# Kernel optimization log

Measured on AMD Instinct MI355X. Metric: run time of the kernel, lower is better.

## Reference

```python
import jax, jax.numpy as jnp
import numpy as np

IN_COUNT = 1024
OUT_COUNT = 1024
NUM_BASIS = 8
INPUT_ABS_MAX = 1.0
X_MIN = 0.0
X_MAX = 1.0
GAMMA_SCALE = 3.0
BATCH = 4096


def setup_inputs() -> dict:
    key = jax.random.key(0)
    k_x, k_c = jax.random.split(key)
    x = jax.random.normal(k_x, (BATCH, IN_COUNT), dtype=jnp.float32)
    coeffs = 0.01 * jax.random.normal(k_c, (OUT_COUNT, IN_COUNT, NUM_BASIS), dtype=jnp.float32)
    # fixed buffers
    centers_1d = jnp.linspace(X_MIN, X_MAX, NUM_BASIS)
    centers = jnp.broadcast_to(centers_1d[None, :], (IN_COUNT, NUM_BASIS)).astype(jnp.float32)
    delta = (X_MAX - X_MIN) / (NUM_BASIS - 1)
    gamma = GAMMA_SCALE / delta
    slopes = jnp.full((IN_COUNT, NUM_BASIS), gamma, dtype=jnp.float32)
    alpha = jnp.full((IN_COUNT,), (X_MAX - X_MIN) / (2.0 * INPUT_ABS_MAX), dtype=jnp.float32)
    beta = jnp.full((IN_COUNT,), 0.5 * (X_MIN + X_MAX), dtype=jnp.float32)
    return {"x": x, "coeffs": coeffs, "centers": centers, "slopes": slopes, "alpha": alpha, "beta": beta}


def reference(x, coeffs, centers, slopes, alpha, beta):
    # u: (B, in) affine transform with fixed alpha/beta
    u = alpha[None, :] * x + beta[None, :]
    # basis: (B, in, basis) = 0.5*(1+tanh(slope*(u - center)))
    basis = 0.5 * (1.0 + jnp.tanh(slopes[None, :, :] * (u[:, :, None] - centers[None, :, :])))
    # y[b,o] = sum_{i,m} coeffs[o,i,m] * basis[b,i,m]  (fused GEMM over in*basis)
    y = jnp.einsum('bim,oim->bo', basis, coeffs)
    return y
```

## Files before the change

kernel.cpp:

```cpp
#include <hip/hip_runtime.h>
#include <hip/hip_bf16.h>
#include <cstdint>
#include <cstddef>

#define BATCH 4096
#define INC   1024
#define OUTC  1024
#define NB    8
#define KDIM  (INC * NB)

#define BM 256
#define BN 256
#define BKB 64
#define SPLITS 4
#define KZ (KDIM / SPLITS)
#define KSTEPS (KZ / BKB)
#define GRID_BLOCKS ((OUTC / BN) * (BATCH / BM) * SPLITS)

#define EXPAND_BLOCKS  ((BATCH * INC) / 256)
#define QUANT_BLOCKS   OUTC
#define PREP_BLOCKS    (EXPAND_BLOCKS + QUANT_BLOCKS)

typedef int   v4i __attribute__((ext_vector_type(4)));
typedef char  v8c __attribute__((ext_vector_type(8)));
typedef short v8s __attribute__((ext_vector_type(8)));

__device__ __forceinline__ unsigned short f2bf(float f) {
  union { float f; unsigned u; } v; v.f = f;
  unsigned r = v.u + 0x7fffu + ((v.u >> 16) & 1u);
  return (unsigned short)(r >> 16);
}
__device__ __forceinline__ float bf2f(unsigned short h) {
  union { unsigned u; float f; } v; v.u = ((unsigned)h) << 16; return v.f;
}

__device__ __forceinline__ void gld16(const char* g, char* l) {
  __builtin_amdgcn_global_load_lds(
      (const __attribute__((address_space(1))) unsigned int*)g,
      (__attribute__((address_space(3))) unsigned int*)l, 16, 0, 0);
}

__global__ __launch_bounds__(256) void prep_kernel(
    const float* __restrict__ x, const float4* __restrict__ coeffs4,
    const float* __restrict__ centers, const float* __restrict__ slopes,
    const float* __restrict__ alpha, const float* __restrict__ beta,
    char* __restrict__ Ai8, int* __restrict__ Ci8i,
    float* __restrict__ maxrow, int* __restrict__ qcsum) {
  const int blk = blockIdx.x;
  const int tid = threadIdx.x;
  if (blk < EXPAND_BLOCKS) {
    const int idx = blk * 256 + tid;
    const int i = idx & (INC - 1);
    const float u = alpha[i] * x[idx] + beta[i];
    const float s0 = slopes[i * NB];
    const float c0 = centers[i * NB];
    const float c1 = centers[i * NB + 1];
    const float L2E2 = 2.8853900817779268f;
    const float a2 = L2E2 * s0;
    float e = __builtin_amdgcn_exp2f(a2 * (c0 - u));
    const float R = __builtin_amdgcn_exp2f(a2 * (c1 - c0));
    v8c q;
#pragma unroll
    for (int m = 0; m < 8; ++m) {
      float basis = __builtin_amdgcn_rcpf(1.0f + e);
      q[m] = (char)(int)rintf(basis * 254.0f - 127.0f);
      e *= R;
    }
    *(v8c*)(Ai8 + (size_t)idx * 8) = q;
  } else {
    const int o = blk - EXPAND_BLOCKS;
    const float4* row = coeffs4 + (size_t)o * (KDIM / 4);
    float4 v[8];
    float m = 0.0f;
#pragma unroll
    for (int j = 0; j < 8; ++j) {
      v[j] = row[tid + 256 * j];
      m = fmaxf(m, fmaxf(fmaxf(fabsf(v[j].x), fabsf(v[j].y)),
                         fmaxf(fabsf(v[j].z), fabsf(v[j].w))));
    }
#pragma unroll
    for (int off = 32; off; off >>= 1) m = fmaxf(m, __shfl_xor(m, off));
    __shared__ float wm[4];
    __shared__ int   wq[4];
    if ((tid & 63) == 0) wm[tid >> 6] = m;
    __syncthreads();
    const float M = fmaxf(fmaxf(fmaxf(wm[0], wm[1]), fmaxf(wm[2], wm[3])), 1e-30f);
    const float s = 127.0f / M;
    int qs = 0;
#pragma unroll
    for (int j = 0; j < 8; ++j) {
      int q0 = (int)rintf(v[j].x * s), q1 = (int)rintf(v[j].y * s);
      int q2 = (int)rintf(v[j].z * s), q3 = (int)rintf(v[j].w * s);
      Ci8i[(size_t)o * (KDIM / 4) + tid + 256 * j] =
          (q0 & 0xFF) | ((q1 & 0xFF) << 8) | ((q2 & 0xFF) << 16) | ((q3 & 0xFF) << 24);
      qs += q0 + q1 + q2 + q3;
    }
#pragma unroll
    for (int off = 32; off; off >>= 1) qs += __shfl_xor(qs, off);
    if ((tid & 63) == 0) wq[tid >> 6] = qs;
    __syncthreads();
    if (tid == 0) { maxrow[o] = M; qcsum[o] = wq[0] + wq[1] + wq[2] + wq[3]; }
  }
}

__global__ __launch_bounds__(512, 2) void gemm_kernel(
    const char* __restrict__ A, const char* __restrict__ C,
    unsigned short* __restrict__ partials) {
  __shared__ __align__(16) char As[3][BM * BKB];
  __shared__ __align__(16) char Bs[3][BN * BKB];

  const int id = (blockIdx.x & 7) * (GRID_BLOCKS / 8) + (blockIdx.x >> 3);
  const int z  = id >> 6;
  const int p  = id & 63;
  const int by = p >> 2;
  const int bx = p & 3;
  const int bm0 = by * BM;
  const int bn0 = bx * BN;
  const int kt0 = z * KZ;

  const int tid  = threadIdx.x;
  const int wave = tid >> 6;
  const int lane = tid & 63;
  const int quad = lane >> 4;
  const int lm   = lane & 15;
  const int wm   = (wave >> 2) * 128;
  const int wn   = (wave & 3) * 64;

  const int r4 = lane >> 2;
  const int gg = (lane & 3) ^ ((lane >> 3) & 3);

  const char* pA0 = A + (size_t)(bm0 + wave * 32 + r4) * KDIM + kt0 + gg * 16;
  const char* pB0 = C + (size_t)(bn0 + wave * 32 + r4) * KDIM + kt0 + gg * 16;
  const int lo = wave * 32 * BKB;

  const int kx   = (quad ^ ((lm >> 1) & 3)) * 16;
  const int aoff = (wm + lm) * BKB + kx;
  const int boff = (wn + lm) * BKB + kx;

  v4i acc[8][4] = {};
  v4i a0v[8], b0v[4], a1v[8], b1v[4];
  int srd = 0;
  int sst = 0;

#define STAGE_NEXT()                                                         \
  {                                                                          \
    _Pragma("unroll")                                                        \
    for (int j = 0; j < 2; ++j) {                                            \
      gld16(pA0 + (size_t)j * (16 * KDIM), As[sst] + lo + j * (16 * BKB));   \
      gld16(pB0 + (size_t)j * (16 * KDIM), Bs[sst] + lo + j * (16 * BKB));   \
    }                                                                        \
    pA0 += BKB; pB0 += BKB;                                                  \
    sst = (sst == 2) ? 0 : sst + 1;                                          \
  }

#define READS(AV, BV)                                                        \
  {                                                                          \
    const char* cA = As[srd] + aoff;                                         \
    const char* cB = Bs[srd] + boff;                                         \
    _Pragma("unroll")                                                        \
    for (int f = 0; f < 8; ++f) AV[f] = *(const v4i*)(cA + f * 16 * BKB);    \
    _Pragma("unroll")                                                        \
    for (int f = 0; f < 4; ++f) BV[f] = *(const v4i*)(cB + f * 16 * BKB);    \
    srd = (srd == 2) ? 0 : srd + 1;                                          \
  }

#define MFMA32(AV, BV)                                                       \
  {                                                                          \
    __builtin_amdgcn_s_setprio(1);                                           \
    _Pragma("unroll")                                                        \
    for (int fm = 0; fm < 8; ++fm)                                           \
      _Pragma("unroll")                                                      \
      for (int fn = 0; fn < 4; ++fn)                                         \
        acc[fm][fn] = __builtin_amdgcn_mfma_i32_16x16x64_i8(AV[fm], BV[fn], acc[fm][fn], 0, 0, 0); \
    __builtin_amdgcn_s_setprio(0);                                           \
  }

#define STEP(CA, CB, NA, NBV, VMS, LGS, DOREADS, DOSTAGE)                    \
  {                                                                          \
    if (DOREADS) {                                                           \
      asm volatile("s_waitcnt vmcnt(" VMS ")" ::: "memory");                 \
      __builtin_amdgcn_sched_barrier(0);                                     \
      __builtin_amdgcn_s_barrier();                                          \
      READS(NA, NBV);                                                        \
    }                                                                        \
    asm volatile("s_waitcnt lgkmcnt(" LGS ")" ::: "memory");                 \
    __builtin_amdgcn_sched_barrier(0);                                       \
    __builtin_amdgcn_s_barrier();                                            \
    if (DOSTAGE) STAGE_NEXT();                                               \
    MFMA32(CA, CB);                                                          \
  }

  STAGE_NEXT(); STAGE_NEXT(); STAGE_NEXT();
  asm volatile("s_waitcnt vmcnt(8)" ::: "memory");
  __builtin_amdgcn_sched_barrier(0);
  __builtin_amdgcn_s_barrier();
  READS(a0v, b0v);

  for (int i = 0; i < 14; ++i) {
    STEP(a0v, b0v, a1v, b1v, "4", "12", true, true);
    STEP(a1v, b1v, a0v, b0v, "4", "12", true, true);
  }
  STEP(a0v, b0v, a1v, b1v, "4", "12", true, true);
  STEP(a1v, b1v, a0v, b0v, "4", "12", true, false);
  STEP(a0v, b0v, a1v, b1v, "0", "12", true, false);
  STEP(a1v, b1v, a0v, b0v, "0", "0",  false, false);
#undef STEP
#undef MFMA32
#undef READS
#undef STAGE_NEXT

  unsigned short* out = partials + (size_t)z * BATCH * OUTC;
#pragma unroll
  for (int fm = 0; fm < 8; ++fm) {
    const int row0 = bm0 + wm + fm * 16 + quad * 4;
#pragma unroll
    for (int fn = 0; fn < 4; ++fn) {
      const int col = bn0 + wn + fn * 16 + lm;
#pragma unroll
      for (int r = 0; r < 4; ++r)
        out[(size_t)(row0 + r) * OUTC + col] = f2bf((float)acc[fm][fn][r]);
    }
  }
}

__global__ __launch_bounds__(256) void reduce_kernel(
    const unsigned short* __restrict__ P, const float* __restrict__ maxrow,
    const int* __restrict__ qcsum, float* __restrict__ out) {
  const size_t nel = (size_t)BATCH * OUTC;
  const size_t base = ((size_t)blockIdx.x * 256 + threadIdx.x) * 8;
  float s[8] = {};
#pragma unroll
  for (int t = 0; t < SPLITS; ++t) {
    v8s v = *(const v8s*)(P + t * nel + base);
#pragma unroll
    for (int j = 0; j < 8; ++j) s[j] += bf2f((unsigned short)v[j]);
  }
  const int o0 = (int)(base & (OUTC - 1));
  const float inv = 1.0f / 32258.0f;
#pragma unroll
  for (int j = 0; j < 8; ++j) {
    const float M = maxrow[o0 + j];
    const int   Q = qcsum[o0 + j];
    s[j] = M * (s[j] + 127.0f * (float)Q) * inv;
  }
  *(float4*)(out + base)     = float4{s[0], s[1], s[2], s[3]};
  *(float4*)(out + base + 4) = float4{s[4], s[5], s[6], s[7]};
}

extern "C" void kernel_launch(void* const* d_in, const int* in_sizes, int n_in,
                              void* d_out, int out_size, void* d_ws, size_t ws_size,
                              hipStream_t stream) {
  const float* x       = (const float*)d_in[0];
  const float* coeffs  = (const float*)d_in[1];
  const float* centers = (const float*)d_in[2];
  const float* slopes  = (const float*)d_in[3];
  const float* alpha   = (const float*)d_in[4];
  const float* beta    = (const float*)d_in[5];
  float* out = (float*)d_out;

  const size_t a_bytes    = (size_t)BATCH * KDIM;
  const size_t c_bytes    = (size_t)OUTC * KDIM;
  const size_t stat_bytes = OUTC * sizeof(float);
  const size_t qcs_bytes  = OUTC * sizeof(int);
  const size_t part_bytes = (size_t)SPLITS * BATCH * OUTC * 2;
  if (ws_size < a_bytes + c_bytes + stat_bytes + qcs_bytes + part_bytes) return;

  char*  Ai8    = (char*)d_ws;
  char*  Ci8    = Ai8 + a_bytes;
  float* maxrow = (float*)(Ci8 + c_bytes);
  int*   qcsum  = (int*)((char*)maxrow + stat_bytes);
  unsigned short* parts = (unsigned short*)((char*)qcsum + qcs_bytes);

  prep_kernel<<<PREP_BLOCKS, 256, 0, stream>>>(
      x, (const float4*)coeffs, centers, slopes, alpha, beta,
      Ai8, (int*)Ci8, maxrow, qcsum);

  gemm_kernel<<<GRID_BLOCKS, 512, 0, stream>>>(Ai8, Ci8, parts);

  reduce_kernel<<<(int)((size_t)BATCH * OUTC / 8 / 256), 256, 0, stream>>>(
      parts, maxrow, qcsum, out);
}
```

Before: 152.8 us.

## Interleave LDS reads and global loads with MFMA quarters; store partials in fragment layout

The GEMM main loop is split into four quarter-steps. Each quarter issues a few LDS fragment reads and one global-to-LDS load, then runs eight MFMAs, with fine-grained lgkmcnt gates and barriers. This is meant to overlap memory traffic with matrix math instead of doing all reads up front. The epilogue now writes bf16 partials in the native accumulator fragment layout as coalesced 16-byte stores, and the reduce kernel is rewritten to read that layout, transpose through shared memory, and write the output coalesced. The extra barriers per step add synchronisation cost, and the reduce grid shrinks to 512 blocks.

```diff
diff --git a/kernel.cpp b/kernel.cpp
--- a/kernel.cpp
+++ b/kernel.cpp
@@ -16,14 +16,15 @@
 #define KZ (KDIM / SPLITS)
 #define KSTEPS (KZ / BKB)
 #define GRID_BLOCKS ((OUTC / BN) * (BATCH / BM) * SPLITS)
+#define FRAG (16 * BKB)
 
 #define EXPAND_BLOCKS  ((BATCH * INC) / 256)
 #define QUANT_BLOCKS   OUTC
 #define PREP_BLOCKS    (EXPAND_BLOCKS + QUANT_BLOCKS)
 
-typedef int   v4i __attribute__((ext_vector_type(4)));
-typedef char  v8c __attribute__((ext_vector_type(8)));
-typedef short v8s __attribute__((ext_vector_type(8)));
+typedef int      v4i __attribute__((ext_vector_type(4)));
+typedef unsigned v4u __attribute__((ext_vector_type(4)));
+typedef char     v8c __attribute__((ext_vector_type(8)));
 
 __device__ __forceinline__ unsigned short f2bf(float f) {
   union { float f; unsigned u; } v; v.f = f;
@@ -105,7 +106,7 @@
 
 __global__ __launch_bounds__(512, 2) void gemm_kernel(
     const char* __restrict__ A, const char* __restrict__ C,
-    unsigned short* __restrict__ partials) {
+    unsigned* __restrict__ partials) {
   __shared__ __align__(16) char As[3][BM * BKB];
   __shared__ __align__(16) char Bs[3][BN * BKB];
 
@@ -138,113 +139,229 @@
   const int boff = (wn + lm) * BKB + kx;
 
   v4i acc[8][4] = {};
-  v4i a0v[8], b0v[4], a1v[8], b1v[4];
+  v4i xa[8], xb[4], ya[8], yb[4];
   int srd = 0;
   int sst = 0;
 
-#define STAGE_NEXT()                                                         \
-  {                                                                          \
-    _Pragma("unroll")                                                        \
-    for (int j = 0; j < 2; ++j) {                                            \
-      gld16(pA0 + (size_t)j * (16 * KDIM), As[sst] + lo + j * (16 * BKB));   \
-      gld16(pB0 + (size_t)j * (16 * KDIM), Bs[sst] + lo + j * (16 * BKB));   \
-    }                                                                        \
+#define STAGE_FULL()                                                         \
+  {                                                                          \
+    gld16(pA0,                     As[sst] + lo);                            \
+    gld16(pA0 + (size_t)16 * KDIM, As[sst] + lo + 16 * BKB);                 \
+    gld16(pB0,                     Bs[sst] + lo);                            \
+    gld16(pB0 + (size_t)16 * KDIM, Bs[sst] + lo + 16 * BKB);                 \
     pA0 += BKB; pB0 += BKB;                                                  \
     sst = (sst == 2) ? 0 : sst + 1;                                          \
   }
 
-#define READS(AV, BV)                                                        \
+#define MFMA8(AS, BS, FM0, FN0)                                              \
+  {                                                                          \
+    __builtin_amdgcn_s_setprio(1);                                           \
+    _Pragma("unroll")                                                        \
+    for (int fm = 0; fm < 4; ++fm)                                           \
+      _Pragma("unroll")                                                      \
+      for (int fn = 0; fn < 2; ++fn)                                         \
+        acc[FM0 + fm][FN0 + fn] = __builtin_amdgcn_mfma_i32_16x16x64_i8(     \
+            AS[FM0 + fm], BS[FN0 + fn], acc[FM0 + fm][FN0 + fn], 0, 0, 0);   \
+    __builtin_amdgcn_s_setprio(0);                                           \
+  }
+
+#define GATE(S)                                                              \
+  asm volatile("s_waitcnt lgkmcnt(" S ")" ::: "memory");                     \
+  __builtin_amdgcn_sched_barrier(0);
+
+#define HALF_MAIN(AX, BX, AY, BY)                                            \
   {                                                                          \
     const char* cA = As[srd] + aoff;                                         \
     const char* cB = Bs[srd] + boff;                                         \
-    _Pragma("unroll")                                                        \
-    for (int f = 0; f < 8; ++f) AV[f] = *(const v4i*)(cA + f * 16 * BKB);    \
-    _Pragma("unroll")                                                        \
-    for (int f = 0; f < 4; ++f) BV[f] = *(const v4i*)(cB + f * 16 * BKB);    \
+                                                                    \
+    AY[0] = *(const v4i*)(cA + 0 * FRAG);                                    \
+    AY[1] = *(const v4i*)(cA + 1 * FRAG);                                    \
+    AY[2] = *(const v4i*)(cA + 2 * FRAG);                                    \
+    gld16(pA0, As[sst] + lo);                                                \
+    asm volatile("s_waitcnt vmcnt(4)" ::: "memory");                         \
+    __builtin_amdgcn_sched_barrier(0);                                       \
+    __builtin_amdgcn_s_barrier();                                            \
+    GATE("3")                                                                \
+    MFMA8(AX, BX, 0, 0)                                                      \
+    __builtin_amdgcn_s_barrier();                                            \
+                                                                    \
+    AY[3] = *(const v4i*)(cA + 3 * FRAG);                                    \
+    BY[0] = *(const v4i*)(cB + 0 * FRAG);                                    \
+    BY[1] = *(const v4i*)(cB + 1 * FRAG);                                    \
+    gld16(pA0 + (size_t)16 * KDIM, As[sst] + lo + 16 * BKB);                 \
+    __builtin_amdgcn_s_barrier();                                            \
+    GATE("6")                                                                \
+    MFMA8(AX, BX, 0, 2)                                                      \
+    __builtin_amdgcn_s_barrier();                                            \
+                                                                    \
+    BY[2] = *(const v4i*)(cB + 2 * FRAG);                                    \
+    BY[3] = *(const v4i*)(cB + 3 * FRAG);                                    \
+    AY[4] = *(const v4i*)(cA + 4 * FRAG);                                    \
+    gld16(pB0, Bs[sst] + lo);                                                \
+    __builtin_amdgcn_s_barrier();                                            \
+    GATE("9")                                                                \
+    MFMA8(AX, BX, 4, 2)                                                      \
+    __builtin_amdgcn_s_barrier();                                            \
+                                                                    \
+    AY[5] = *(const v4i*)(cA + 5 * FRAG);                                    \
+    AY[6] = *(const v4i*)(cA + 6 * FRAG);                                    \
+    AY[7] = *(const v4i*)(cA + 7 * FRAG);                                    \
+    gld16(pB0 + (size_t)16 * KDIM, Bs[sst] + lo + 16 * BKB);                 \
+    __builtin_amdgcn_s_barrier();                                            \
+    GATE("0")                                                                \
+    MFMA8(AX, BX, 4, 0)                                                      \
+    __builtin_amdgcn_s_barrier();                                            \
+    pA0 += BKB; pB0 += BKB;                                                  \
+    sst = (sst == 2) ? 0 : sst + 1;                                          \
     srd = (srd == 2) ? 0 : srd + 1;                                          \
   }
 
-#define MFMA32(AV, BV)                                                       \
-  {                                                                          \
-    __builtin_amdgcn_s_setprio(1);                                           \
-    _Pragma("unroll")                                                        \
-    for (int fm = 0; fm < 8; ++fm)                                           \
-      _Pragma("unroll")                                                      \
-      for (int fn = 0; fn < 4; ++fn)                                         \
-        acc[fm][fn] = __builtin_amdgcn_mfma_i32_16x16x64_i8(AV[fm], BV[fn], acc[fm][fn], 0, 0, 0); \
-    __builtin_amdgcn_s_setprio(0);                                           \
-  }
-
-#define STEP(CA, CB, NA, NBV, VMS, LGS, DOREADS, DOSTAGE)                    \
-  {                                                                          \
-    if (DOREADS) {                                                           \
-      asm volatile("s_waitcnt vmcnt(" VMS ")" ::: "memory");                 \
-      __builtin_amdgcn_sched_barrier(0);                                     \
-      __builtin_amdgcn_s_barrier();                                          \
-      READS(NA, NBV);                                                        \
-    }                                                                        \
-    asm volatile("s_waitcnt lgkmcnt(" LGS ")" ::: "memory");                 \
+#define HALF_NOST(AX, BX, AY, BY, VMS)                                       \
+  {                                                                          \
+    const char* cA = As[srd] + aoff;                                         \
+    const char* cB = Bs[srd] + boff;                                         \
+    AY[0] = *(const v4i*)(cA + 0 * FRAG);                                    \
+    AY[1] = *(const v4i*)(cA + 1 * FRAG);                                    \
+    AY[2] = *(const v4i*)(cA + 2 * FRAG);                                    \
+    asm volatile("s_waitcnt vmcnt(" VMS ")" ::: "memory");                   \
     __builtin_amdgcn_sched_barrier(0);                                       \
     __builtin_amdgcn_s_barrier();                                            \
-    if (DOSTAGE) STAGE_NEXT();                                               \
-    MFMA32(CA, CB);                                                          \
-  }
-
-  STAGE_NEXT(); STAGE_NEXT(); STAGE_NEXT();
+    GATE("3")                                                                \
+    MFMA8(AX, BX, 0, 0)                                                      \
+    __builtin_amdgcn_s_barrier();                                            \
+    AY[3] = *(const v4i*)(cA + 3 * FRAG);                                    \
+    BY[0] = *(const v4i*)(cB + 0 * FRAG);                                    \
+    BY[1] = *(const v4i*)(cB + 1 * FRAG);                                    \
+    __builtin_amdgcn_s_barrier();                                            \
+    GATE("6")                                                                \
+    MFMA8(AX, BX, 0, 2)                                                      \
+    __builtin_amdgcn_s_barrier();                                            \
+    BY[2] = *(const v4i*)(cB + 2 * FRAG);                                    \
+    BY[3] = *(const v4i*)(cB + 3 * FRAG);                                    \
+    AY[4] = *(const v4i*)(cA + 4 * FRAG);                                    \
+    __builtin_amdgcn_s_barrier();                                            \
+    GATE("9")                                                                \
+    MFMA8(AX, BX, 4, 2)                                                      \
+    __builtin_amdgcn_s_barrier();                                            \
+    AY[5] = *(const v4i*)(cA + 5 * FRAG);                                    \
+    AY[6] = *(const v4i*)(cA + 6 * FRAG);                                    \
+    AY[7] = *(const v4i*)(cA + 7 * FRAG);                                    \
+    __builtin_amdgcn_s_barrier();                                            \
+    GATE("0")                                                                \
+    MFMA8(AX, BX, 4, 0)                                                      \
+    __builtin_amdgcn_s_barrier();                                            \
+    srd = (srd == 2) ? 0 : srd + 1;                                          \
+  }
+
+#define HALF_FIN(AX, BX)                                                     \
+  {                                                                          \
+    GATE("0")                                                                \
+    MFMA8(AX, BX, 0, 0)                                                      \
+    MFMA8(AX, BX, 0, 2)                                                      \
+    MFMA8(AX, BX, 4, 2)                                                      \
+    MFMA8(AX, BX, 4, 0)                                                      \
+  }
+
+  STAGE_FULL(); STAGE_FULL(); STAGE_FULL();
   asm volatile("s_waitcnt vmcnt(8)" ::: "memory");
   __builtin_amdgcn_sched_barrier(0);
   __builtin_amdgcn_s_barrier();
-  READS(a0v, b0v);
+  {
+    const char* cA = As[0] + aoff;
+    const char* cB = Bs[0] + boff;
+#pragma unroll
+    for (int f = 0; f < 8; ++f) xa[f] = *(const v4i*)(cA + f * FRAG);
+#pragma unroll
+    for (int f = 0; f < 4; ++f) xb[f] = *(const v4i*)(cB + f * FRAG);
+  }
+  srd = 1;
 
   for (int i = 0; i < 14; ++i) {
-    STEP(a0v, b0v, a1v, b1v, "4", "12", true, true);
-    STEP(a1v, b1v, a0v, b0v, "4", "12", true, true);
-  }
-  STEP(a0v, b0v, a1v, b1v, "4", "12", true, true);
-  STEP(a1v, b1v, a0v, b0v, "4", "12", true, false);
-  STEP(a0v, b0v, a1v, b1v, "0", "12", true, false);
-  STEP(a1v, b1v, a0v, b0v, "0", "0",  false, false);
-#undef STEP
-#undef MFMA32
-#undef READS
-#undef STAGE_NEXT
-
-  unsigned short* out = partials + (size_t)z * BATCH * OUTC;
-#pragma unroll
-  for (int fm = 0; fm < 8; ++fm) {
-    const int row0 = bm0 + wm + fm * 16 + quad * 4;
-#pragma unroll
-    for (int fn = 0; fn < 4; ++fn) {
-      const int col = bn0 + wn + fn * 16 + lm;
-#pragma unroll
-      for (int r = 0; r < 4; ++r)
-        out[(size_t)(row0 + r) * OUTC + col] = f2bf((float)acc[fm][fn][r]);
-    }
-  }
+    HALF_MAIN(xa, xb, ya, yb);
+    HALF_MAIN(ya, yb, xa, xb);
+  }
+  HALF_MAIN(xa, xb, ya, yb);
+  HALF_NOST(ya, yb, xa, xb, "4");
+  HALF_NOST(xa, xb, ya, yb, "0");
+  HALF_FIN(ya, yb);
+#undef HALF_FIN
+#undef HALF_NOST
+#undef HALF_MAIN
+#undef GATE
+#undef MFMA8
+#undef STAGE_FULL
+
+  unsigned w32[64];
+#pragma unroll
+  for (int fm = 0; fm < 8; ++fm)
+#pragma unroll
+    for (int fn = 0; fn < 4; ++fn)
+#pragma unroll
+      for (int rr = 0; rr < 2; ++rr)
+        w32[fm * 8 + fn * 2 + rr] =
+            (unsigned)f2bf((float)acc[fm][fn][2 * rr]) |
+            ((unsigned)f2bf((float)acc[fm][fn][2 * rr + 1]) << 16);
+
+  unsigned* outp = partials + (((size_t)z * 64 + p) * 8 + wave) * 4096 + lane * 4;
+#pragma unroll
+  for (int c = 0; c < 16; ++c)
+    *(v4u*)(outp + c * 256) = v4u{w32[4 * c], w32[4 * c + 1], w32[4 * c + 2], w32[4 * c + 3]};
 }
 
 __global__ __launch_bounds__(256) void reduce_kernel(
-    const unsigned short* __restrict__ P, const float* __restrict__ maxrow,
+    const unsigned* __restrict__ P, const float* __restrict__ maxrow,
     const int* __restrict__ qcsum, float* __restrict__ out) {
-  const size_t nel = (size_t)BATCH * OUTC;
-  const size_t base = ((size_t)blockIdx.x * 256 + threadIdx.x) * 8;
-  float s[8] = {};
-#pragma unroll
-  for (int t = 0; t < SPLITS; ++t) {
-    v8s v = *(const v8s*)(P + t * nel + base);
-#pragma unroll
-    for (int j = 0; j < 8; ++j) s[j] += bf2f((unsigned short)v[j]);
-  }
-  const int o0 = (int)(base & (OUTC - 1));
+  const int blk = blockIdx.x;
+  const int p = blk >> 3, w = blk & 7;
+  const int by = p >> 2, bx = p & 3;
+  const int B0 = by * BM + (w >> 2) * 128;
+  const int O0 = bx * BN + (w & 3) * 64;
+  const int t = threadIdx.x;
+  const int l = t & 63;
+
+  __shared__ float tile[128][65];
+  __shared__ float sM[64];
+  __shared__ float sQ[64];
+  if (t < 64) { sM[t] = maxrow[O0 + t]; sQ[t] = 127.0f * (float)qcsum[O0 + t]; }
+  __syncthreads();
+
+  const size_t region = ((size_t)p * 8 + w) * 4096;
+  const size_t zs     = (size_t)64 * 8 * 4096;
+  float slo[16] = {}, shi[16] = {};
+#pragma unroll
+  for (int z = 0; z < SPLITS; ++z) {
+#pragma unroll
+    for (int r = 0; r < 4; ++r) {
+      v4u u = *(const v4u*)(P + z * zs + region + ((t >> 6) + r * 4) * 256 + l * 4);
+#pragma unroll
+      for (int i = 0; i < 4; ++i) {
+        slo[r * 4 + i] += bf2f((unsigned short)(u[i] & 0xFFFFu));
+        shi[r * 4 + i] += bf2f((unsigned short)(u[i] >> 16));
+      }
+    }
+  }
   const float inv = 1.0f / 32258.0f;
 #pragma unroll
-  for (int j = 0; j < 8; ++j) {
-    const float M = maxrow[o0 + j];
-    const int   Q = qcsum[o0 + j];
-    s[j] = M * (s[j] + 127.0f * (float)Q) * inv;
-  }
-  *(float4*)(out + base)     = float4{s[0], s[1], s[2], s[3]};
-  *(float4*)(out + base + 4) = float4{s[4], s[5], s[6], s[7]};
+  for (int r = 0; r < 4; ++r)
+#pragma unroll
+    for (int i = 0; i < 4; ++i) {
+      const int jj = (t >> 6) * 4 + r * 16 + i;
+      const int fm = jj >> 3, fn = (jj >> 1) & 3, rr = jj & 1;
+      const int bl = fm * 16 + (l >> 4) * 4 + rr * 2;
+      const int ol = fn * 16 + (l & 15);
+      const float M = sM[ol], corr = sQ[ol];
+      tile[bl][ol]     = M * (slo[r * 4 + i] + corr) * inv;
+      tile[bl + 1][ol] = M * (shi[r * 4 + i] + corr) * inv;
+    }
+  __syncthreads();
+
+  const int row = t >> 1;
+  const int c0  = (t & 1) * 32;
+  float* op = out + (size_t)(B0 + row) * OUTC + O0 + c0;
+#pragma unroll
+  for (int i = 0; i < 8; ++i)
+    *(float4*)(op + 4 * i) = float4{tile[row][c0 + 4 * i],     tile[row][c0 + 4 * i + 1],
+                                    tile[row][c0 + 4 * i + 2], tile[row][c0 + 4 * i + 3]};
 }
 
 extern "C" void kernel_launch(void* const* d_in, const int* in_sizes, int n_in,
@@ -269,7 +386,7 @@
   char*  Ci8    = Ai8 + a_bytes;
   float* maxrow = (float*)(Ci8 + c_bytes);
   int*   qcsum  = (int*)((char*)maxrow + stat_bytes);
-  unsigned short* parts = (unsigned short*)((char*)qcsum + qcs_bytes);
+  unsigned* parts = (unsigned*)((char*)qcsum + qcs_bytes);
 
   prep_kernel<<<PREP_BLOCKS, 256, 0, stream>>>(
       x, (const float4*)coeffs, centers, slopes, alpha, beta,
@@ -277,6 +394,5 @@
 
   gemm_kernel<<<GRID_BLOCKS, 512, 0, stream>>>(Ai8, Ci8, parts);
 
-  reduce_kernel<<<(int)((size_t)BATCH * OUTC / 8 / 256), 256, 0, stream>>>(
-      parts, maxrow, qcsum, out);
-}
+  reduce_kernel<<<64 * 8, 256, 0, stream>>>(parts, maxrow, qcsum, out);
+}
```

After: 157.3 us. 2.9% more time.
